# Kernel optimization log

Measured on AMD Instinct MI355X. Metric: run time of the kernel, lower is better.

The kernel has to match this reference:

```python
import jax, jax.numpy as jnp
import numpy as np

N = 100_000      # nodes
E = 1_600_000    # edges (avg degree 16)
D = 128          # emb_dim == hidden_dim
OUT = 128        # out_dim
NUM_BOND_TYPE = 6
NUM_BOND_DIR = 3


def _xavier(key, fan_in, fan_out, shape):
    a = np.sqrt(6.0 / (fan_in + fan_out)).astype(np.float32)
    return jax.random.uniform(key, shape, jnp.float32, -a, a)


def setup_inputs() -> dict:
    key = jax.random.key(0)
    ks = jax.random.split(key, 12)
    x = jax.random.normal(ks[0], (N, D), jnp.float32)
    edge_index = jax.random.randint(ks[1], (2, E), 0, N)
    edge_attr = jax.random.randint(ks[2], (E, 2), 0, NUM_BOND_DIR)
    # PReLU single learnable slope (torch init 0.25)
    prelu_a = jnp.full((1,), 0.25, jnp.float32)
    # enc_to_dec: Linear(D, D, bias=False), torch default uniform(-1/sqrt(D), 1/sqrt(D))
    s = 1.0 / np.sqrt(D)
    W_enc = jax.random.uniform(ks[3], (D, D), jnp.float32, -s, s)
    # edge embedding tables, xavier_uniform
    emb1 = _xavier(ks[4], NUM_BOND_TYPE, D, (NUM_BOND_TYPE, D))
    emb2 = _xavier(ks[5], NUM_BOND_DIR, D, (NUM_BOND_DIR, D))
    # GIN MLP: Linear(D, 2D) -> ReLU -> Linear(2D, OUT)
    W1 = jax.random.uniform(ks[6], (2 * D, D), jnp.float32, -s, s)
    b1 = jax.random.uniform(ks[7], (2 * D,), jnp.float32, -s, s)
    s2 = 1.0 / np.sqrt(2 * D)
    W2 = jax.random.uniform(ks[8], (OUT, 2 * D), jnp.float32, -s2, s2)
    b2 = jax.random.uniform(ks[9], (OUT,), jnp.float32, -s2, s2)
    return {
        "x": x, "edge_index": edge_index, "edge_attr": edge_attr,
        "prelu_a": prelu_a, "W_enc": W_enc,
        "emb1": emb1, "emb2": emb2,
        "W1": W1, "b1": b1, "W2": W2, "b2": b2,
    }


def reference(x, edge_index, edge_attr, prelu_a, W_enc, emb1, emb2, W1, b1, W2, b2):
    # PReLU then enc_to_dec (no bias)
    h = jnp.where(x >= 0, x, prelu_a * x)          # [N, D]
    h = h @ W_enc.T                                 # [N, D]
    src, dst = edge_index[0], edge_index[1]
    # edge embeddings for real edges
    e_emb = emb1[edge_attr[:, 0]] + emb2[edge_attr[:, 1]]  # [E, D]
    # messages: x_j + edge_attr, scatter-add at dst
    msg = h[src] + e_emb                             # [E, D]
    agg = jax.ops.segment_sum(msg, dst, num_segments=N)    # [N, D]
    # self-loops: appended edge (i, i) with attr [4, 0]
    self_emb = emb1[4] + emb2[0]                     # [D]
    agg = agg + h + self_emb[None, :]
    # GIN update MLP
    hid = jax.nn.relu(agg @ W1.T + b1)               # [N, 2D]
    out = hid @ W2.T + b2                            # [N, OUT]
    return out
```

## Files before the change

kernel.cpp:

```cpp
#include <hip/hip_runtime.h>
#include <hip/hip_bf16.h>

#define DD 128

typedef short bf16x8 __attribute__((ext_vector_type(8)));
typedef float f32x4 __attribute__((ext_vector_type(4)));

__device__ __forceinline__ float bf2f_lo(unsigned int u) {
    union { unsigned int v; float f; } x; x.v = u << 16; return x.f;
}
__device__ __forceinline__ float bf2f_hi(unsigned int u) {
    union { unsigned int v; float f; } x; x.v = u & 0xFFFF0000u; return x.f;
}
__device__ __forceinline__ unsigned short f2bf(float f) {
    union { float f; unsigned int u; } x; x.f = f;
    unsigned int u = x.u;
    unsigned int r = (u + 0x7FFFu + ((u >> 16) & 1u)) >> 16;
    return (unsigned short)r;
}

#define SBSH 7
#define SBN  128
#define NBP  256
#define NSBMAX 800
#define PKCAP 4096

__global__ __launch_bounds__(256) void wcvt_k(const float* __restrict__ Wenc,
                                              const float* __restrict__ W1,
                                              const float* __restrict__ W2,
                                              unsigned short* __restrict__ wb) {
    int i = (blockIdx.x * 256 + threadIdx.x) * 4;
    if (i >= 81920) return;
    const float* src;
    int off;
    if (i < 16384)      { src = Wenc; off = 0; }
    else if (i < 49152) { src = W1;   off = 16384; }
    else                { src = W2;   off = 49152; }
    float4 v = *(const float4*)&src[i - off];
    ushort4 w;
    w.x = f2bf(v.x); w.y = f2bf(v.y); w.z = f2bf(v.z); w.w = f2bf(v.w);
    *(ushort4*)&wb[i] = w;
}

__global__ __launch_bounds__(256) void sbhist_k(const int* __restrict__ ei,
                                                int* __restrict__ bh,
                                                int E, int chunk, int nsb) {
    __shared__ int h4[4][NSBMAX];
    int wid = threadIdx.x >> 6;
    for (int i = threadIdx.x; i < 4 * NSBMAX; i += 256) ((int*)h4)[i] = 0;
    __syncthreads();
    int b = blockIdx.x;
    int beg = b * chunk, end = min(E, beg + chunk);
    for (int e = beg + threadIdx.x; e < end; e += 256)
        atomicAdd(&h4[wid][ei[E + e] >> SBSH], 1);
    __syncthreads();
    for (int i = threadIdx.x; i < nsb; i += 256)
        bh[i * NBP + b] = h4[0][i] + h4[1][i] + h4[2][i] + h4[3][i];
}

__global__ __launch_bounds__(256) void pscan1_k(const int* __restrict__ bh,
                                                int* __restrict__ bsum, int ntot) {
    __shared__ int ws[4];
    int base = blockIdx.x * 2048 + threadIdx.x * 8;
    int s = 0;
    #pragma unroll
    for (int i = 0; i < 8; ++i) { int idx = base + i; if (idx < ntot) s += bh[idx]; }
    int lane = threadIdx.x & 63, wid = threadIdx.x >> 6;
    int ss = s;
    #pragma unroll
    for (int o = 1; o < 64; o <<= 1) { int t = __shfl_up(ss, o, 64); if (lane >= o) ss += t; }
    if (lane == 63) ws[wid] = ss;
    __syncthreads();
    if (threadIdx.x == 0) bsum[blockIdx.x] = ws[0] + ws[1] + ws[2] + ws[3];
}

__global__ void pscan2_k(int* __restrict__ bsum, int nb) {
    if (threadIdx.x == 0 && blockIdx.x == 0) {
        int c = 0;
        for (int i = 0; i < nb; ++i) { int t = bsum[i]; bsum[i] = c; c += t; }
    }
}

__global__ __launch_bounds__(256) void pscan3_k(const int* __restrict__ bh,
                                                const int* __restrict__ bsum,
                                                int* __restrict__ bho, int ntot) {
    __shared__ int ws[4];
    int base = blockIdx.x * 2048 + threadIdx.x * 8;
    int v[8]; int s = 0;
    #pragma unroll
    for (int i = 0; i < 8; ++i) { int idx = base + i; v[i] = (idx < ntot) ? bh[idx] : 0; s += v[i]; }
    int lane = threadIdx.x & 63, wid = threadIdx.x >> 6;
    int ss = s;
    #pragma unroll
    for (int o = 1; o < 64; o <<= 1) { int t = __shfl_up(ss, o, 64); if (lane >= o) ss += t; }
    if (lane == 63) ws[wid] = ss;
    __syncthreads();
    if (threadIdx.x == 0) { int c = 0; for (int w = 0; w < 4; ++w) { int t = ws[w]; ws[w] = c; c += t; } }
    __syncthreads();
    int excl = ss - s + ws[wid] + bsum[blockIdx.x];
    #pragma unroll
    for (int i = 0; i < 8; ++i) {
        int idx = base + i;
        if (idx < ntot) bho[idx] = excl;
        excl += v[i];
    }
}

__global__ __launch_bounds__(256) void part_k(const int* __restrict__ ei,
                                              const int* __restrict__ ea,
                                              const int* __restrict__ bho,
                                              int* __restrict__ rec,
                                              int E, int chunk, int nsb) {
    __shared__ int cur[NSBMAX];
    int b = blockIdx.x;
    for (int i = threadIdx.x; i < nsb; i += 256) cur[i] = bho[i * NBP + b];
    __syncthreads();
    int beg = b * chunk, end = min(E, beg + chunk);
    for (int e = beg + threadIdx.x; e < end; e += 256) {
        int src = ei[e];
        int dst = ei[E + e];
        int2 aa = *(const int2*)&ea[2 * e];
        int pos = atomicAdd(&cur[dst >> SBSH], 1);
        rec[pos] = src | ((aa.x * 3 + aa.y) << 17) | ((dst & (SBN - 1)) << 21);
    }
}

__global__ __launch_bounds__(256) void gemm1_k(
    const float* __restrict__ Ap, const unsigned short* __restrict__ Wb,
    unsigned short* __restrict__ Hb,
    const float* __restrict__ prelu_a, int M)
{
    const int K = 128;
    const int tid = threadIdx.x;
    const int wid = tid >> 6, lane = tid & 63;
    const float pa = prelu_a[0];

    const int r0 = blockIdx.x * 128 + wid * 32;
    const int rl = lane & 15, kb = (lane >> 4) * 8;

    bf16x8 af[2][4];
    #pragma unroll
    for (int rf = 0; rf < 2; ++rf) {
        int row = r0 + rf * 16 + rl; if (row > M - 1) row = M - 1;
        #pragma unroll
        for (int kf = 0; kf < 4; ++kf) {
            float4 v0 = *(const float4*)&Ap[(size_t)row * K + kf * 32 + kb];
            float4 v1 = *(const float4*)&Ap[(size_t)row * K + kf * 32 + kb + 4];
            v0.x = v0.x >= 0.f ? v0.x : pa * v0.x;
            v0.y = v0.y >= 0.f ? v0.y : pa * v0.y;
            v0.z = v0.z >= 0.f ? v0.z : pa * v0.z;
            v0.w = v0.w >= 0.f ? v0.w : pa * v0.w;
            v1.x = v1.x >= 0.f ? v1.x : pa * v1.x;
            v1.y = v1.y >= 0.f ? v1.y : pa * v1.y;
            v1.z = v1.z >= 0.f ? v1.z : pa * v1.z;
            v1.w = v1.w >= 0.f ? v1.w : pa * v1.w;
            bf16x8 t;
            t[0] = (short)f2bf(v0.x); t[1] = (short)f2bf(v0.y);
            t[2] = (short)f2bf(v0.z); t[3] = (short)f2bf(v0.w);
            t[4] = (short)f2bf(v1.x); t[5] = (short)f2bf(v1.y);
            t[6] = (short)f2bf(v1.z); t[7] = (short)f2bf(v1.w);
            af[rf][kf] = t;
        }
    }

    f32x4 acc[8][2];
    const f32x4 zz = {0.f, 0.f, 0.f, 0.f};
    #pragma unroll
    for (int nt = 0; nt < 8; ++nt) { acc[nt][0] = zz; acc[nt][1] = zz; }

    #pragma unroll
    for (int nt = 0; nt < 8; ++nt) {
        bf16x8 bf[4];
        #pragma unroll
        for (int kf = 0; kf < 4; ++kf)
            bf[kf] = *(const bf16x8*)&Wb[(size_t)(nt * 16 + rl) * K + kf * 32 + kb];
        #pragma unroll
        for (int rf = 0; rf < 2; ++rf)
            #pragma unroll
            for (int kf = 0; kf < 4; ++kf)
                acc[nt][rf] = __builtin_amdgcn_mfma_f32_16x16x32_bf16(af[rf][kf], bf[kf], acc[nt][rf], 0, 0, 0);
    }

    const int rq = (lane >> 4) * 4;
    #pragma unroll
    for (int nt = 0; nt < 8; ++nt) {
        int c = nt * 16 + rl;
        #pragma unroll
        for (int rf = 0; rf < 2; ++rf) {
            int rb = r0 + rf * 16 + rq;
            #pragma unroll
            for (int t = 0; t < 4; ++t) {
                int r = rb + t;
                if (r < M) Hb[(size_t)r * 128 + c] = f2bf(acc[nt][rf][t]);
            }
        }
    }
}

__global__ __launch_bounds__(1024) void csragg_k(
    const unsigned short* __restrict__ h,
    const int* __restrict__ rec,
    const int* __restrict__ bho,
    const float* __restrict__ emb1, const float* __restrict__ emb2,
    int* __restrict__ packed, unsigned int* __restrict__ aggb,
    int nsb, int M, int E)
{
    __shared__ float emb12[10][DD];
    __shared__ int hist[SBN];
    __shared__ int lstart[SBN];
    __shared__ int wsum[2];
    __shared__ int pkl[PKCAP];
    const int s = blockIdx.x;
    const int t = threadIdx.x;
    const int lane = t & 63, wid = t >> 6;

    for (int i = t; i < 10 * DD; i += 1024) {
        int c = i >> 7, col = i & 127;
        float v;
        if (c == 9) v = emb1[4 * DD + col] + emb2[col];
        else        v = emb1[(c / 3) * DD + col] + emb2[(c % 3) * DD + col];
        emb12[c][col] = v;
    }
    int sb0 = bho[s * NBP];
    int sb1 = (s == nsb - 1) ? E : bho[(s + 1) * NBP];
    if (t < SBN) hist[t] = 0;
    __syncthreads();

    const bool inlds = (sb1 - sb0) <= PKCAP;

    for (int i = sb0 + t; i < sb1; i += 1024)
        atomicAdd(&hist[(rec[i] >> 21) & (SBN - 1)], 1);
    __syncthreads();

    int v = (t < SBN) ? hist[t] : 0;
    int ss = v;
    #pragma unroll
    for (int o = 1; o < 64; o <<= 1) { int u = __shfl_up(ss, o, 64); if (lane >= o) ss += u; }
    if (t < SBN && lane == 63) wsum[wid] = ss;
    __syncthreads();
    if (t == 0) { int c = 0; for (int w = 0; w < 2; ++w) { int x2 = wsum[w]; wsum[w] = c; c += x2; } }
    __syncthreads();
    if (t < SBN) {
        lstart[t] = ss - v + wsum[wid];
        hist[t] = 0;
    }
    __syncthreads();

    if (inlds) {
        for (int i = sb0 + t; i < sb1; i += 1024) {
            int r = rec[i];
            int dl = (r >> 21) & (SBN - 1);
            int pos = lstart[dl] + atomicAdd(&hist[dl], 1);
            pkl[pos] = r & 0x1FFFFF;
        }
    } else {
        for (int i = sb0 + t; i < sb1; i += 1024) {
            int r = rec[i];
            int dl = (r >> 21) & (SBN - 1);
            int pos = sb0 + lstart[dl] + atomicAdd(&hist[dl], 1);
            packed[pos] = r & 0x1FFFFF;
        }
    }
    __syncthreads();

    const int n0 = s << SBSH;
    const int c2 = lane * 2;
    #pragma unroll
    for (int k = 0; k < SBN / 16; ++k) {
        int r = wid + k * 16;
        int n = n0 + r;
        if (n >= M) continue;
        int lbeg = lstart[r];
        int lend = lbeg + hist[r];
        unsigned int hn = *(const unsigned int*)&h[(size_t)n * DD + c2];
        float2 acc = {bf2f_lo(hn) + emb12[9][c2], bf2f_hi(hn) + emb12[9][c2 + 1]};
        if (inlds) {
            int e = lbeg;
            for (; e + 8 <= lend; e += 8) {
                int p[8]; unsigned int hv[8]; float2 m[8];
                #pragma unroll
                for (int i = 0; i < 8; ++i) p[i] = pkl[e + i];
                #pragma unroll
                for (int i = 0; i < 8; ++i)
                    hv[i] = *(const unsigned int*)&h[(size_t)(p[i] & 0x1FFFF) * DD + c2];
                #pragma unroll
                for (int i = 0; i < 8; ++i)
                    m[i] = *(const float2*)&emb12[(p[i] >> 17) & 15][c2];
                #pragma unroll
                for (int i = 0; i < 8; ++i) {
                    acc.x += bf2f_lo(hv[i]) + m[i].x;
                    acc.y += bf2f_hi(hv[i]) + m[i].y;
                }
            }
            for (; e < lend; ++e) {
                int p = pkl[e];
                unsigned int hv = *(const unsigned int*)&h[(size_t)(p & 0x1FFFF) * DD + c2];
                float2 m = *(const float2*)&emb12[(p >> 17) & 15][c2];
                acc.x += bf2f_lo(hv) + m.x;
                acc.y += bf2f_hi(hv) + m.y;
            }
        } else {
            int e = sb0 + lbeg, end = sb0 + lend;
            for (; e + 8 <= end; e += 8) {
                int p[8]; unsigned int hv[8]; float2 m[8];
                #pragma unroll
                for (int i = 0; i < 8; ++i) p[i] = packed[e + i];
                #pragma unroll
                for (int i = 0; i < 8; ++i)
                    hv[i] = *(const unsigned int*)&h[(size_t)(p[i] & 0x1FFFF) * DD + c2];
                #pragma unroll
                for (int i = 0; i < 8; ++i)
                    m[i] = *(const float2*)&emb12[(p[i] >> 17) & 15][c2];
                #pragma unroll
                for (int i = 0; i < 8; ++i) {
                    acc.x += bf2f_lo(hv[i]) + m[i].x;
                    acc.y += bf2f_hi(hv[i]) + m[i].y;
                }
            }
            for (; e < end; ++e) {
                int p = packed[e];
                unsigned int hv = *(const unsigned int*)&h[(size_t)(p & 0x1FFFF) * DD + c2];
                float2 m = *(const float2*)&emb12[(p >> 17) & 15][c2];
                acc.x += bf2f_lo(hv) + m.x;
                acc.y += bf2f_hi(hv) + m.y;
            }
        }
        aggb[((size_t)n * DD + c2) >> 1] = ((unsigned int)f2bf(acc.y) << 16) | f2bf(acc.x);
    }
}

__global__ __launch_bounds__(512) void mlp_k(
    const unsigned short* __restrict__ A,
    const unsigned short* __restrict__ w1b,
    const float* __restrict__ b1,
    const unsigned short* __restrict__ w2b,
    const float* __restrict__ b2,
    float* __restrict__ out, int M)
{
    __shared__ unsigned short W1l[256][136];
    __shared__ unsigned short hidl[128][264];
    unsigned short (*W2l)[264] = (unsigned short (*)[264])&W1l[0][0];

    const int tid = threadIdx.x;
    const int wid = tid >> 6, lane = tid & 63;
    const int rl = lane & 15, kb = (lane >> 4) * 8;
    const int rq = (lane >> 4) * 4;
    const int r0 = blockIdx.x * 128;

    #pragma unroll
    for (int idx = tid; idx < 256 * 16; idx += 512) {
        int n = idx >> 4, kq = idx & 15;
        *(ushort4*)&W1l[n][kq * 8] = *(const ushort4*)&w1b[(size_t)n * 128 + kq * 8];
        *(ushort4*)&W1l[n][kq * 8 + 4] = *(const ushort4*)&w1b[(size_t)n * 128 + kq * 8 + 4];
    }
    bf16x8 af[4];
    {
        int row = r0 + wid * 16 + rl; if (row > M - 1) row = M - 1;
        #pragma unroll
        for (int kf = 0; kf < 4; ++kf)
            af[kf] = *(const bf16x8*)&A[(size_t)row * 128 + kf * 32 + kb];
    }
    __syncthreads();

    f32x4 acc1[16];
    const f32x4 zz = {0.f, 0.f, 0.f, 0.f};
    #pragma unroll
    for (int nt = 0; nt < 16; ++nt) acc1[nt] = zz;
    #pragma unroll
    for (int nt = 0; nt < 16; ++nt) {
        bf16x8 bf[4];
        #pragma unroll
        for (int kf = 0; kf < 4; ++kf)
            bf[kf] = *(const bf16x8*)&W1l[nt * 16 + rl][kf * 32 + kb];
        #pragma unroll
        for (int kf = 0; kf < 4; ++kf)
            acc1[nt] = __builtin_amdgcn_mfma_f32_16x16x32_bf16(af[kf], bf[kf], acc1[nt], 0, 0, 0);
    }
    #pragma unroll
    for (int nt = 0; nt < 16; ++nt) {
        int c = nt * 16 + rl;
        float bi = b1[c];
        #pragma unroll
        for (int t = 0; t < 4; ++t)
            hidl[wid * 16 + rq + t][c] = f2bf(fmaxf(acc1[nt][t] + bi, 0.f));
    }
    __syncthreads();

    #pragma unroll
    for (int idx = tid; idx < 128 * 32; idx += 512) {
        int n = idx >> 5, kq = idx & 31;
        *(ushort4*)&W2l[n][kq * 8] = *(const ushort4*)&w2b[(size_t)n * 256 + kq * 8];
        *(ushort4*)&W2l[n][kq * 8 + 4] = *(const ushort4*)&w2b[(size_t)n * 256 + kq * 8 + 4];
    }
    __syncthreads();

    bf16x8 af2[8];
    #pragma unroll
    for (int kf = 0; kf < 8; ++kf)
        af2[kf] = *(const bf16x8*)&hidl[wid * 16 + rl][kf * 32 + kb];
    f32x4 acc2[8];
    #pragma unroll
    for (int nt = 0; nt < 8; ++nt) acc2[nt] = zz;
    #pragma unroll
    for (int nt = 0; nt < 8; ++nt) {
        bf16x8 bf[8];
        #pragma unroll
        for (int kf = 0; kf < 8; ++kf)
            bf[kf] = *(const bf16x8*)&W2l[nt * 16 + rl][kf * 32 + kb];
        #pragma unroll
        for (int kf = 0; kf < 8; ++kf)
            acc2[nt] = __builtin_amdgcn_mfma_f32_16x16x32_bf16(af2[kf], bf[kf], acc2[nt], 0, 0, 0);
    }
    #pragma unroll
    for (int nt = 0; nt < 8; ++nt) {
        int c = nt * 16 + rl;
        float bi = b2[c];
        #pragma unroll
        for (int t = 0; t < 4; ++t) {
            int r = r0 + wid * 16 + rq + t;
            if (r < M) out[(size_t)r * 128 + c] = acc2[nt][t] + bi;
        }
    }
}

extern "C" void kernel_launch(void* const* d_in, const int* in_sizes, int n_in,
                              void* d_out, int out_size, void* d_ws, size_t ws_size,
                              hipStream_t stream) {
    const float* x     = (const float*)d_in[0];
    const int*   ei    = (const int*)d_in[1];
    const int*   ea    = (const int*)d_in[2];
    const float* pa    = (const float*)d_in[3];
    const float* Wenc  = (const float*)d_in[4];
    const float* emb1  = (const float*)d_in[5];
    const float* emb2  = (const float*)d_in[6];
    const float* W1    = (const float*)d_in[7];
    const float* b1    = (const float*)d_in[8];
    const float* W2    = (const float*)d_in[9];
    const float* b2    = (const float*)d_in[10];
    float* out = (float*)d_out;

    const int M = in_sizes[0] / DD;
    const int E = in_sizes[1] / 2;
    const int nsb = (M + SBN - 1) >> SBSH;
    const int chunk = (E + NBP - 1) / NBP;
    const int ntot = nsb * NBP;
    const int nscb = (ntot + 2047) / 2048;

    char* ws = (char*)d_ws;
    size_t o = 0;
    unsigned short* h_bf  = (unsigned short*)(ws + o); o += (size_t)M * DD * 2;
    unsigned int*   aggb  = (unsigned int*)(ws + o);   o += (size_t)M * DD * 2;
    int* rec    = (int*)(ws + o); o += (size_t)E * 4;
    int* packed = (int*)(ws + o); o += (size_t)E * 4;
    int* bh     = (int*)(ws + o); o += (size_t)ntot * 4;
    int* bho    = (int*)(ws + o); o += (size_t)ntot * 4;
    int* bsum   = (int*)(ws + o); o += (size_t)nscb * 4;
    unsigned short* wb = (unsigned short*)(ws + o); o += 81920 * 2;
    unsigned short* wenc_b = wb;
    unsigned short* w1_b   = wb + 16384;
    unsigned short* w2_b   = wb + 49152;

    const int gm = (M + 127) / 128;
    dim3 blk(256);

    wcvt_k<<<dim3(80), blk, 0, stream>>>(Wenc, W1, W2, wb);

    sbhist_k<<<dim3(NBP), blk, 0, stream>>>(ei, bh, E, chunk, nsb);
    pscan1_k<<<dim3(nscb), blk, 0, stream>>>(bh, bsum, ntot);
    pscan2_k<<<dim3(1), dim3(64), 0, stream>>>(bsum, nscb);
    pscan3_k<<<dim3(nscb), blk, 0, stream>>>(bh, bsum, bho, ntot);
    part_k<<<dim3(NBP), blk, 0, stream>>>(ei, ea, bho, rec, E, chunk, nsb);

    gemm1_k<<<dim3(gm), blk, 0, stream>>>(x, wenc_b, h_bf, pa, M);

    csragg_k<<<dim3(nsb), dim3(1024), 0, stream>>>(
        h_bf, rec, bho, emb1, emb2, packed, aggb, nsb, M, E);

    mlp_k<<<dim3(gm), dim3(512), 0, stream>>>(
        (const unsigned short*)aggb, w1_b, b1, w2_b, b2, out, M);
}
```

Measured before the change: 205.2 us.

## Merge preprocessing kernels and fold block-offset scan into pscan3

Fuses the weight conversion into the destination histogram kernel as extra blocks, and fuses edge partitioning with the first GEMM in one launch using block-index ranges. It also removes the single-thread serial scan kernel: each pscan3 block now computes its own offset by reducing the preceding block sums. This cuts the launch count from eight to five and lets the partition and GEMM work overlap, at the cost of heterogeneous blocks that may balance unevenly. The reduction assumes the number of scan blocks is at most 256.

```diff
diff --git a/kernel.cpp b/kernel.cpp
--- a/kernel.cpp
+++ b/kernel.cpp
@@ -25,11 +25,27 @@
 #define NSBMAX 800
 #define PKCAP 4096
 
-__global__ __launch_bounds__(256) void wcvt_k(const float* __restrict__ Wenc,
-                                              const float* __restrict__ W1,
-                                              const float* __restrict__ W2,
-                                              unsigned short* __restrict__ wb) {
-    int i = (blockIdx.x * 256 + threadIdx.x) * 4;
+__global__ __launch_bounds__(256) void sbwc_k(
+    const int* __restrict__ ei, int* __restrict__ bh,
+    const float* __restrict__ Wenc, const float* __restrict__ W1,
+    const float* __restrict__ W2, unsigned short* __restrict__ wb,
+    int E, int chunk, int nsb)
+{
+    __shared__ int h4[4][NSBMAX];
+    const int b = blockIdx.x;
+    if (b < NBP) {
+        int wid = threadIdx.x >> 6;
+        for (int i = threadIdx.x; i < 4 * NSBMAX; i += 256) ((int*)h4)[i] = 0;
+        __syncthreads();
+        int beg = b * chunk, end = min(E, beg + chunk);
+        for (int e = beg + threadIdx.x; e < end; e += 256)
+            atomicAdd(&h4[wid][ei[E + e] >> SBSH], 1);
+        __syncthreads();
+        for (int i = threadIdx.x; i < nsb; i += 256)
+            bh[i * NBP + b] = h4[0][i] + h4[1][i] + h4[2][i] + h4[3][i];
+        return;
+    }
+    int i = ((b - NBP) * 256 + threadIdx.x) * 4;
     if (i >= 81920) return;
     const float* src;
     int off;
@@ -42,22 +58,6 @@
     *(ushort4*)&wb[i] = w;
 }
 
-__global__ __launch_bounds__(256) void sbhist_k(const int* __restrict__ ei,
-                                                int* __restrict__ bh,
-                                                int E, int chunk, int nsb) {
-    __shared__ int h4[4][NSBMAX];
-    int wid = threadIdx.x >> 6;
-    for (int i = threadIdx.x; i < 4 * NSBMAX; i += 256) ((int*)h4)[i] = 0;
-    __syncthreads();
-    int b = blockIdx.x;
-    int beg = b * chunk, end = min(E, beg + chunk);
-    for (int e = beg + threadIdx.x; e < end; e += 256)
-        atomicAdd(&h4[wid][ei[E + e] >> SBSH], 1);
-    __syncthreads();
-    for (int i = threadIdx.x; i < nsb; i += 256)
-        bh[i * NBP + b] = h4[0][i] + h4[1][i] + h4[2][i] + h4[3][i];
-}
-
 __global__ __launch_bounds__(256) void pscan1_k(const int* __restrict__ bh,
                                                 int* __restrict__ bsum, int ntot) {
     __shared__ int ws[4];
@@ -74,30 +74,35 @@
     if (threadIdx.x == 0) bsum[blockIdx.x] = ws[0] + ws[1] + ws[2] + ws[3];
 }
 
-__global__ void pscan2_k(int* __restrict__ bsum, int nb) {
-    if (threadIdx.x == 0 && blockIdx.x == 0) {
-        int c = 0;
-        for (int i = 0; i < nb; ++i) { int t = bsum[i]; bsum[i] = c; c += t; }
-    }
-}
-
 __global__ __launch_bounds__(256) void pscan3_k(const int* __restrict__ bh,
                                                 const int* __restrict__ bsum,
                                                 int* __restrict__ bho, int ntot) {
     __shared__ int ws[4];
-    int base = blockIdx.x * 2048 + threadIdx.x * 8;
+    __shared__ int boff;
+    const int b = blockIdx.x;
+    const int t = threadIdx.x;
+    const int lane = t & 63, wid = t >> 6;
+
+    int pv = (t < b) ? bsum[t] : 0;
+    #pragma unroll
+    for (int o = 32; o; o >>= 1) pv += __shfl_xor(pv, o, 64);
+    if (lane == 0) ws[wid] = pv;
+    __syncthreads();
+    if (t == 0) boff = ws[0] + ws[1] + ws[2] + ws[3];
+    __syncthreads();
+
+    int base = b * 2048 + t * 8;
     int v[8]; int s = 0;
     #pragma unroll
     for (int i = 0; i < 8; ++i) { int idx = base + i; v[i] = (idx < ntot) ? bh[idx] : 0; s += v[i]; }
-    int lane = threadIdx.x & 63, wid = threadIdx.x >> 6;
     int ss = s;
     #pragma unroll
-    for (int o = 1; o < 64; o <<= 1) { int t = __shfl_up(ss, o, 64); if (lane >= o) ss += t; }
+    for (int o = 1; o < 64; o <<= 1) { int u = __shfl_up(ss, o, 64); if (lane >= o) ss += u; }
     if (lane == 63) ws[wid] = ss;
     __syncthreads();
-    if (threadIdx.x == 0) { int c = 0; for (int w = 0; w < 4; ++w) { int t = ws[w]; ws[w] = c; c += t; } }
-    __syncthreads();
-    int excl = ss - s + ws[wid] + bsum[blockIdx.x];
+    if (t == 0) { int c = 0; for (int w = 0; w < 4; ++w) { int u = ws[w]; ws[w] = c; c += u; } }
+    __syncthreads();
+    int excl = ss - s + ws[wid] + boff;
     #pragma unroll
     for (int i = 0; i < 8; ++i) {
         int idx = base + i;
@@ -106,36 +111,35 @@
     }
 }
 
-__global__ __launch_bounds__(256) void part_k(const int* __restrict__ ei,
-                                              const int* __restrict__ ea,
-                                              const int* __restrict__ bho,
-                                              int* __restrict__ rec,
-                                              int E, int chunk, int nsb) {
+__global__ __launch_bounds__(256) void pg_k(
+    const int* __restrict__ ei, const int* __restrict__ ea,
+    const int* __restrict__ bho, int* __restrict__ rec,
+    const float* __restrict__ x, const unsigned short* __restrict__ Wb,
+    unsigned short* __restrict__ Hb, const float* __restrict__ prelu_a,
+    int E, int chunk, int nsb, int M)
+{
     __shared__ int cur[NSBMAX];
-    int b = blockIdx.x;
-    for (int i = threadIdx.x; i < nsb; i += 256) cur[i] = bho[i * NBP + b];
-    __syncthreads();
-    int beg = b * chunk, end = min(E, beg + chunk);
-    for (int e = beg + threadIdx.x; e < end; e += 256) {
-        int src = ei[e];
-        int dst = ei[E + e];
-        int2 aa = *(const int2*)&ea[2 * e];
-        int pos = atomicAdd(&cur[dst >> SBSH], 1);
-        rec[pos] = src | ((aa.x * 3 + aa.y) << 17) | ((dst & (SBN - 1)) << 21);
-    }
-}
-
-__global__ __launch_bounds__(256) void gemm1_k(
-    const float* __restrict__ Ap, const unsigned short* __restrict__ Wb,
-    unsigned short* __restrict__ Hb,
-    const float* __restrict__ prelu_a, int M)
-{
+    const int tid = threadIdx.x;
+
+    if (blockIdx.x < NBP) {
+        int b = blockIdx.x;
+        for (int i = tid; i < nsb; i += 256) cur[i] = bho[i * NBP + b];
+        __syncthreads();
+        int beg = b * chunk, end = min(E, beg + chunk);
+        for (int e = beg + tid; e < end; e += 256) {
+            int src = ei[e];
+            int dst = ei[E + e];
+            int2 aa = *(const int2*)&ea[2 * e];
+            int pos = atomicAdd(&cur[dst >> SBSH], 1);
+            rec[pos] = src | ((aa.x * 3 + aa.y) << 17) | ((dst & (SBN - 1)) << 21);
+        }
+        return;
+    }
+
     const int K = 128;
-    const int tid = threadIdx.x;
     const int wid = tid >> 6, lane = tid & 63;
     const float pa = prelu_a[0];
-
-    const int r0 = blockIdx.x * 128 + wid * 32;
+    const int r0 = (blockIdx.x - NBP) * 128 + wid * 32;
     const int rl = lane & 15, kb = (lane >> 4) * 8;
 
     bf16x8 af[2][4];
@@ -144,8 +148,8 @@
         int row = r0 + rf * 16 + rl; if (row > M - 1) row = M - 1;
         #pragma unroll
         for (int kf = 0; kf < 4; ++kf) {
-            float4 v0 = *(const float4*)&Ap[(size_t)row * K + kf * 32 + kb];
-            float4 v1 = *(const float4*)&Ap[(size_t)row * K + kf * 32 + kb + 4];
+            float4 v0 = *(const float4*)&x[(size_t)row * K + kf * 32 + kb];
+            float4 v1 = *(const float4*)&x[(size_t)row * K + kf * 32 + kb + 4];
             v0.x = v0.x >= 0.f ? v0.x : pa * v0.x;
             v0.y = v0.y >= 0.f ? v0.y : pa * v0.y;
             v0.z = v0.z >= 0.f ? v0.z : pa * v0.z;
@@ -463,15 +467,13 @@
     const int gm = (M + 127) / 128;
     dim3 blk(256);
 
-    wcvt_k<<<dim3(80), blk, 0, stream>>>(Wenc, W1, W2, wb);
-
-    sbhist_k<<<dim3(NBP), blk, 0, stream>>>(ei, bh, E, chunk, nsb);
+    sbwc_k<<<dim3(NBP + 80), blk, 0, stream>>>(ei, bh, Wenc, W1, W2, wb, E, chunk, nsb);
+
     pscan1_k<<<dim3(nscb), blk, 0, stream>>>(bh, bsum, ntot);
-    pscan2_k<<<dim3(1), dim3(64), 0, stream>>>(bsum, nscb);
     pscan3_k<<<dim3(nscb), blk, 0, stream>>>(bh, bsum, bho, ntot);
-    part_k<<<dim3(NBP), blk, 0, stream>>>(ei, ea, bho, rec, E, chunk, nsb);
-
-    gemm1_k<<<dim3(gm), blk, 0, stream>>>(x, wenc_b, h_bf, pa, M);
+
+    pg_k<<<dim3(NBP + gm), blk, 0, stream>>>(
+        ei, ea, bho, rec, x, wenc_b, h_bf, pa, E, chunk, nsb, M);
 
     csragg_k<<<dim3(nsb), dim3(1024), 0, stream>>>(
         h_bf, rec, bho, emb1, emb2, packed, aggb, nsb, M, E);
```

Measured after the change: 187.2 us. 1.1x faster.
